# Kernel tuning notes

Measured on AMD Instinct MI355X. Metric: run time of the kernel, lower is better.

The kernel has to match this reference:

```python
import jax, jax.numpy as jnp
import numpy as np

B, C, H, W = 8, 512, 64, 64
GH, GW = 240, 240  # hardcoded grid size in the source (240*240*2 slice)


def bilinear_grid_sample(x, grid):
    """F.grid_sample equivalent: bilinear, zeros padding, align_corners=True
    (old-PyTorch default used by this repo).
    x: [b, c, H, W], grid: [b, Hg, Wg, 2] with (x, y) normalized coords in [-1, 1].
    """
    b, c, h, w = x.shape
    hg, wg = grid.shape[1], grid.shape[2]
    ix = (grid[..., 0] + 1.0) * 0.5 * (w - 1)  # unnormalize, align_corners=True
    iy = (grid[..., 1] + 1.0) * 0.5 * (h - 1)
    ix0 = jnp.floor(ix)
    iy0 = jnp.floor(iy)
    ix1 = ix0 + 1.0
    iy1 = iy0 + 1.0
    wx1 = ix - ix0
    wx0 = 1.0 - wx1
    wy1 = iy - iy0
    wy0 = 1.0 - wy1
    xf = x.transpose(0, 2, 3, 1).reshape(b, h * w, c)  # [b, HW, c]

    def gather(iy_, ix_):
        m = (iy_ >= 0) & (iy_ <= h - 1) & (ix_ >= 0) & (ix_ <= w - 1)
        iyc = jnp.clip(iy_, 0, h - 1).astype(jnp.int32)
        ixc = jnp.clip(ix_, 0, w - 1).astype(jnp.int32)
        idx = (iyc * w + ixc).reshape(b, hg * wg, 1)
        v = jnp.take_along_axis(xf, idx, axis=1).reshape(b, hg, wg, c)
        return v * m[..., None].astype(x.dtype)

    out = (gather(iy0, ix0) * (wy0 * wx0)[..., None]
           + gather(iy0, ix1) * (wy0 * wx1)[..., None]
           + gather(iy1, ix0) * (wy1 * wx0)[..., None]
           + gather(iy1, ix1) * (wy1 * wx1)[..., None])
    return out.transpose(0, 3, 1, 2)  # [b, c, Hg, Wg]


def _identity_grid(b, h, w, dtype):
    # GeometricTnf resize == grid_sample with identity affine grid (align_corners=True)
    ys = jnp.linspace(-1.0, 1.0, h, dtype=dtype)
    xs = jnp.linspace(-1.0, 1.0, w, dtype=dtype)
    gy, gx = jnp.meshgrid(ys, xs, indexing='ij')
    return jnp.broadcast_to(jnp.stack([gx, gy], axis=-1)[None], (b, h, w, 2))


def setup_inputs() -> dict:
    key = jax.random.key(0)
    # grid channels must hold normalized coords, so sample uniform in [-1, 1]
    data = jax.random.uniform(key, (B, C, H, W), dtype=jnp.float32, minval=-1.0, maxval=1.0)
    return {"data": data}


def reference(data) -> jnp.ndarray:
    b, c, h, w = data.shape
    x = data[:, :c - 256]            # [b, c-256, h, w]
    theta_aff = data[:, c - 256:c - 128]
    theta_aff_tps = data[:, c - 128:]
    g_aff = theta_aff.reshape(b, -1)[:, :GH * GW * 2].reshape(b, GH, GW, 2)
    g_tps = theta_aff_tps.reshape(b, -1)[:, :GH * GW * 2].reshape(b, GH, GW, 2)
    warped_aff = bilinear_grid_sample(x, g_aff)          # [b, cx, 240, 240]
    warped_aff_tps = bilinear_grid_sample(warped_aff, g_tps)  # [b, cx, 240, 240]
    resized = bilinear_grid_sample(warped_aff_tps, _identity_grid(b, h, w, data.dtype))
    return x + resized
```

## Files before the change

kernel.cpp:

```cpp
#include <hip/hip_runtime.h>

#define H 64
#define W 64
#define NPIX 4096
#define GHH 240
#define GWW 240
#define CB 512
#define CX 256
#define NTAP 64
#define NT4  16

static __device__ __forceinline__ unsigned pk_bf16(float a, float b) {
    unsigned ua = __float_as_uint(a);
    ua = (ua + 0x7fffu + ((ua >> 16) & 1u)) >> 16;
    unsigned ub = __float_as_uint(b);
    ub = (ub + 0x7fffu + ((ub >> 16) & 1u)) & 0xffff0000u;
    return ua | ub;
}
static __device__ __forceinline__ float lo_bf16(unsigned u) { return __uint_as_float(u << 16); }
static __device__ __forceinline__ float hi_bf16(unsigned u) { return __uint_as_float(u & 0xffff0000u); }
static __device__ __forceinline__ unsigned pk_wi(float w, unsigned idx) {
    unsigned ub = __float_as_uint(w);
    ub = (ub + 0x7fffu + ((ub >> 16) & 1u)) & 0xffff0000u;
    return ub | idx;
}

__global__ __launch_bounds__(64)
void stencil_kernel(const float* __restrict__ data, uint4* __restrict__ st) {
    const int gid = blockIdx.x * 64 + threadIdx.x;
    const int b   = gid & 7;
    const int pix = gid >> 3;
    const int oy = pix >> 6, ox = pix & 63;

    const float*  xbase = data + (size_t)b * CB * NPIX;
    const float2* gaff  = (const float2*)(xbase + (size_t)256 * NPIX);
    const float2* gtps  = (const float2*)(xbase + (size_t)384 * NPIX);
    uint4* stb = st + (size_t)b * NT4 * NPIX;

    const float fy  = ((float)oy / 63.0f) * 239.0f;
    const float fx  = ((float)ox / 63.0f) * 239.0f;
    const float fy0 = floorf(fy), fx0 = floorf(fx);
    const float wy1 = fy - fy0,  wx1 = fx - fx0;

#pragma unroll
    for (int t = 0; t < 4; ++t) {
        const int tty = t >> 1, ttx = t & 1;
        const float gyf = fy0 + (float)tty;
        const float gxf = fx0 + (float)ttx;
        float wt = (tty ? wy1 : 1.0f - wy1) * (ttx ? wx1 : 1.0f - wx1);
        if (gyf < 0.0f || gyf > 239.0f || gxf < 0.0f || gxf > 239.0f) wt = 0.0f;
        const int gyi = min(max((int)gyf, 0), GHH - 1);
        const int gxi = min(max((int)gxf, 0), GWW - 1);

        const float2 gt = gtps[gyi * GWW + gxi];
        const float sx  = (gt.x + 1.0f) * 0.5f * 239.0f;
        const float sy  = (gt.y + 1.0f) * 0.5f * 239.0f;
        const float sy0 = floorf(sy), sx0 = floorf(sx);
        const float wsy1 = sy - sy0,  wsx1 = sx - sx0;

#pragma unroll
        for (int s = 0; s < 4; ++s) {
            const int ssy = s >> 1, ssx = s & 1;
            const float ayf = sy0 + (float)ssy;
            const float axf = sx0 + (float)ssx;
            float ws = (ssy ? wsy1 : 1.0f - wsy1) * (ssx ? wsx1 : 1.0f - wsx1);
            if (ayf < 0.0f || ayf > 239.0f || axf < 0.0f || axf > 239.0f) ws = 0.0f;
            ws *= wt;
            const int ayi = min(max((int)ayf, 0), GHH - 1);
            const int axi = min(max((int)axf, 0), GWW - 1);

            const float2 ga = gaff[ayi * GWW + axi];
            const float qx  = (ga.x + 1.0f) * 0.5f * 63.0f;
            const float qy  = (ga.y + 1.0f) * 0.5f * 63.0f;
            const float qy0 = floorf(qy), qx0 = floorf(qx);
            const float wqy1 = qy - qy0,  wqx1 = qx - qx0;

            unsigned pk[4];
#pragma unroll
            for (int r = 0; r < 4; ++r) {
                const int rry = r >> 1, rrx = r & 1;
                const float byf = qy0 + (float)rry;
                const float bxf = qx0 + (float)rrx;
                float wr = (rry ? wqy1 : 1.0f - wqy1) * (rrx ? wqx1 : 1.0f - wqx1);
                if (byf < 0.0f || byf > 63.0f || bxf < 0.0f || bxf > 63.0f) wr = 0.0f;
                wr *= ws;
                const int byi = min(max((int)byf, 0), H - 1);
                const int bxi = min(max((int)bxf, 0), W - 1);
                pk[r] = pk_wi(wr, (unsigned)(byi * W + bxi));
            }
            stb[(size_t)(t * 4 + s) * NPIX + pix] = make_uint4(pk[0], pk[1], pk[2], pk[3]);
        }
    }
}

__global__ __launch_bounds__(1024)
void gather_kernel(const float* __restrict__ data, const uint4* __restrict__ st,
                   float* __restrict__ out) {
    __shared__ uint4 xl[NPIX];
    const int tid  = threadIdx.x;
    const int b    = blockIdx.x & 7;
    const int cg   = (blockIdx.x >> 3) & 31;
    const int half = blockIdx.x >> 8;
    const int c0   = cg * 8;

    const float* xbase = data + (size_t)b * CB * NPIX;
    const float* xc    = xbase + (size_t)c0 * NPIX;

#pragma unroll
    for (int k = 0; k < 4; ++k) {
        const int p = k * 1024 + tid;
        float v0 = xc[0 * NPIX + p], v1 = xc[1 * NPIX + p];
        float v2 = xc[2 * NPIX + p], v3 = xc[3 * NPIX + p];
        float v4 = xc[4 * NPIX + p], v5 = xc[5 * NPIX + p];
        float v6 = xc[6 * NPIX + p], v7 = xc[7 * NPIX + p];
        uint4 u;
        u.x = pk_bf16(v0, v1); u.y = pk_bf16(v2, v3);
        u.z = pk_bf16(v4, v5); u.w = pk_bf16(v6, v7);
        xl[p] = u;
    }
    __syncthreads();

    const uint4* stb = st + (size_t)b * NT4 * NPIX;

#pragma unroll
    for (int pg = 0; pg < 2; ++pg) {
        const int pix = half * 2048 + pg * 1024 + tid;
        float a0 = 0.f, a1 = 0.f, a2 = 0.f, a3 = 0.f;
        float a4 = 0.f, a5 = 0.f, a6 = 0.f, a7 = 0.f;

#pragma unroll 4
        for (int g = 0; g < NT4; ++g) {
            const uint4 s4 = stb[(size_t)g * NPIX + pix];
#pragma unroll
            for (int r = 0; r < 4; ++r) {
                const unsigned u = (&s4.x)[r];
                const float w = __uint_as_float(u & 0xffff0000u);
                const uint4 v = xl[u & 0xffffu];
                a0 = fmaf(w, lo_bf16(v.x), a0); a1 = fmaf(w, hi_bf16(v.x), a1);
                a2 = fmaf(w, lo_bf16(v.y), a2); a3 = fmaf(w, hi_bf16(v.y), a3);
                a4 = fmaf(w, lo_bf16(v.z), a4); a5 = fmaf(w, hi_bf16(v.z), a5);
                a6 = fmaf(w, lo_bf16(v.w), a6); a7 = fmaf(w, hi_bf16(v.w), a7);
            }
        }

        float* o = out + ((size_t)b * CX + c0) * NPIX + pix;
        o[0 * NPIX] = xc[0 * NPIX + pix] + a0;
        o[1 * NPIX] = xc[1 * NPIX + pix] + a1;
        o[2 * NPIX] = xc[2 * NPIX + pix] + a2;
        o[3 * NPIX] = xc[3 * NPIX + pix] + a3;
        o[4 * NPIX] = xc[4 * NPIX + pix] + a4;
        o[5 * NPIX] = xc[5 * NPIX + pix] + a5;
        o[6 * NPIX] = xc[6 * NPIX + pix] + a6;
        o[7 * NPIX] = xc[7 * NPIX + pix] + a7;
    }
}

__global__ __launch_bounds__(1024, 4)
void warp_resblock_mono(const float* __restrict__ data, float* __restrict__ out) {
    const int tid = threadIdx.x;
    const int b   = blockIdx.x & 7;
    const int cg  = blockIdx.x >> 3;
    const int c0  = cg * 8;

    const float*  xbase = data + (size_t)b * CB * NPIX;
    const float2* gaff  = (const float2*)(xbase + (size_t)256 * NPIX);
    const float2* gtps  = (const float2*)(xbase + (size_t)384 * NPIX);

    __shared__ float4 xa[NPIX];
    __shared__ float4 xb[NPIX];
    {
        const float4* xs = (const float4*)(xbase + (size_t)c0 * NPIX);
        float4 va[4], vb[4];
#pragma unroll
        for (int cc = 0; cc < 4; ++cc) va[cc] = xs[(size_t)cc * 1024 + tid];
#pragma unroll
        for (int cc = 0; cc < 4; ++cc) vb[cc] = xs[(size_t)(4 + cc) * 1024 + tid];
#pragma unroll
        for (int k = 0; k < 4; ++k) {
            const int pix = tid * 4 + k;
            xa[pix] = make_float4(((const float*)&va[0])[k], ((const float*)&va[1])[k],
                                  ((const float*)&va[2])[k], ((const float*)&va[3])[k]);
            xb[pix] = make_float4(((const float*)&vb[0])[k], ((const float*)&vb[1])[k],
                                  ((const float*)&vb[2])[k], ((const float*)&vb[3])[k]);
        }
    }
    __syncthreads();

    for (int pg = 0; pg < 4; ++pg) {
        const int pix = pg * 1024 + tid;
        const int oy = pix >> 6, ox = pix & 63;
        float a0 = 0.f, a1 = 0.f, a2 = 0.f, a3 = 0.f;
        float a4 = 0.f, a5 = 0.f, a6 = 0.f, a7 = 0.f;

        const float fy  = ((float)oy / 63.0f) * 239.0f;
        const float fx  = ((float)ox / 63.0f) * 239.0f;
        const float fy0 = floorf(fy), fx0 = floorf(fx);
        const float wy1 = fy - fy0,  wx1 = fx - fx0;

#pragma unroll
        for (int t = 0; t < 4; ++t) {
            const int tty = t >> 1, ttx = t & 1;
            const float gyf = fy0 + (float)tty;
            const float gxf = fx0 + (float)ttx;
            float wt = (tty ? wy1 : 1.0f - wy1) * (ttx ? wx1 : 1.0f - wx1);
            if (gyf < 0.0f || gyf > 239.0f || gxf < 0.0f || gxf > 239.0f) wt = 0.0f;
            const int gyi = min(max((int)gyf, 0), GHH - 1);
            const int gxi = min(max((int)gxf, 0), GWW - 1);
            const float2 gt = gtps[gyi * GWW + gxi];
            const float sx  = (gt.x + 1.0f) * 0.5f * 239.0f;
            const float sy  = (gt.y + 1.0f) * 0.5f * 239.0f;
            const float sy0 = floorf(sy), sx0 = floorf(sx);
            const float wsy1 = sy - sy0,  wsx1 = sx - sx0;
#pragma unroll
            for (int s = 0; s < 4; ++s) {
                const int ssy = s >> 1, ssx = s & 1;
                const float ayf = sy0 + (float)ssy;
                const float axf = sx0 + (float)ssx;
                float ws = (ssy ? wsy1 : 1.0f - wsy1) * (ssx ? wsx1 : 1.0f - wsx1);
                if (ayf < 0.0f || ayf > 239.0f || axf < 0.0f || axf > 239.0f) ws = 0.0f;
                ws *= wt;
                const int ayi = min(max((int)ayf, 0), GHH - 1);
                const int axi = min(max((int)axf, 0), GWW - 1);
                const float2 ga = gaff[ayi * GWW + axi];
                const float qx  = (ga.x + 1.0f) * 0.5f * 63.0f;
                const float qy  = (ga.y + 1.0f) * 0.5f * 63.0f;
                const float qy0 = floorf(qy), qx0 = floorf(qx);
                const float wqy1 = qy - qy0,  wqx1 = qx - qx0;
#pragma unroll
                for (int r = 0; r < 4; ++r) {
                    const int rry = r >> 1, rrx = r & 1;
                    const float byf = qy0 + (float)rry;
                    const float bxf = qx0 + (float)rrx;
                    float wr = (rry ? wqy1 : 1.0f - wqy1) * (rrx ? wqx1 : 1.0f - wqx1);
                    if (byf < 0.0f || byf > 63.0f || bxf < 0.0f || bxf > 63.0f) wr = 0.0f;
                    wr *= ws;
                    const int byi = min(max((int)byf, 0), H - 1);
                    const int bxi = min(max((int)bxf, 0), W - 1);
                    const int idx = byi * W + bxi;
                    const float4 pa = xa[idx];
                    const float4 pb = xb[idx];
                    a0 = fmaf(wr, pa.x, a0); a1 = fmaf(wr, pa.y, a1);
                    a2 = fmaf(wr, pa.z, a2); a3 = fmaf(wr, pa.w, a3);
                    a4 = fmaf(wr, pb.x, a4); a5 = fmaf(wr, pb.y, a5);
                    a6 = fmaf(wr, pb.z, a6); a7 = fmaf(wr, pb.w, a7);
                }
            }
        }
        const float4 ra = xa[pix];
        const float4 rb = xb[pix];
        float* o = out + ((size_t)b * CX + c0) * NPIX + pix;
        o[0 * NPIX] = ra.x + a0; o[1 * NPIX] = ra.y + a1;
        o[2 * NPIX] = ra.z + a2; o[3 * NPIX] = ra.w + a3;
        o[4 * NPIX] = rb.x + a4; o[5 * NPIX] = rb.y + a5;
        o[6 * NPIX] = rb.z + a6; o[7 * NPIX] = rb.w + a7;
    }
}

extern "C" void kernel_launch(void* const* d_in, const int* in_sizes, int n_in,
                              void* d_out, int out_size, void* d_ws, size_t ws_size,
                              hipStream_t stream) {
    (void)in_sizes; (void)n_in; (void)out_size;
    const float* data = (const float*)d_in[0];
    float* out = (float*)d_out;
    const size_t ws_needed = (size_t)8 * NT4 * NPIX * sizeof(uint4);

    if (ws_size >= ws_needed) {
        uint4* st = (uint4*)d_ws;
        hipLaunchKernelGGL(stencil_kernel, dim3(512), dim3(64), 0, stream, data, st);
        hipLaunchKernelGGL(gather_kernel, dim3(512), dim3(1024), 0, stream, data, st, out);
    } else {
        hipLaunchKernelGGL(warp_resblock_mono, dim3(256), dim3(1024), 0, stream, data, out);
    }
}
```

Before: 53.44 us.

## Vectorize gather loads, process two pixels per thread, nontemporal stores

The stencil kernel moves to 256-thread blocks with each block covering one batch. The gather kernel now loads channel data with float4 vector reads when filling LDS, and each thread accumulates two adjacent pixels at once, which doubles independent LDS gathers in flight. Outputs are written as float2 nontemporal stores, and a launch bound hints at 8 waves per SIMD. The goal is more memory-level parallelism and wider transactions. In exchange, register pressure rises from 16 accumulators, and the stencil loads become strided by two pixels.

New measurement: 55.19 us. 1.03x slower.

```diff
diff --git a/kernel.cpp b/kernel.cpp
--- a/kernel.cpp
+++ b/kernel.cpp
@@ -7,8 +7,9 @@
 #define GWW 240
 #define CB 512
 #define CX 256
-#define NTAP 64
 #define NT4  16
+
+typedef float f32x2 __attribute__((ext_vector_type(2)));
 
 static __device__ __forceinline__ unsigned pk_bf16(float a, float b) {
     unsigned ua = __float_as_uint(a);
@@ -25,11 +26,10 @@
     return ub | idx;
 }
 
-__global__ __launch_bounds__(64)
+__global__ __launch_bounds__(256)
 void stencil_kernel(const float* __restrict__ data, uint4* __restrict__ st) {
-    const int gid = blockIdx.x * 64 + threadIdx.x;
-    const int b   = gid & 7;
-    const int pix = gid >> 3;
+    const int b   = blockIdx.x & 7;
+    const int pix = (blockIdx.x >> 3) * 256 + threadIdx.x;
     const int oy = pix >> 6, ox = pix & 63;
 
     const float*  xbase = data + (size_t)b * CB * NPIX;
@@ -93,7 +93,7 @@
     }
 }
 
-__global__ __launch_bounds__(1024)
+__global__ __launch_bounds__(1024, 8)
 void gather_kernel(const float* __restrict__ data, const uint4* __restrict__ st,
                    float* __restrict__ out) {
     __shared__ uint4 xl[NPIX];
@@ -106,52 +106,61 @@
     const float* xbase = data + (size_t)b * CB * NPIX;
     const float* xc    = xbase + (size_t)c0 * NPIX;
 
-#pragma unroll
-    for (int k = 0; k < 4; ++k) {
-        const int p = k * 1024 + tid;
-        float v0 = xc[0 * NPIX + p], v1 = xc[1 * NPIX + p];
-        float v2 = xc[2 * NPIX + p], v3 = xc[3 * NPIX + p];
-        float v4 = xc[4 * NPIX + p], v5 = xc[5 * NPIX + p];
-        float v6 = xc[6 * NPIX + p], v7 = xc[7 * NPIX + p];
-        uint4 u;
-        u.x = pk_bf16(v0, v1); u.y = pk_bf16(v2, v3);
-        u.z = pk_bf16(v4, v5); u.w = pk_bf16(v6, v7);
-        xl[p] = u;
+    {
+        float4 va[8];
+#pragma unroll
+        for (int c = 0; c < 8; ++c)
+            va[c] = ((const float4*)(xc + (size_t)c * NPIX))[tid];
+#pragma unroll
+        for (int k = 0; k < 4; ++k) {
+            uint4 u;
+            u.x = pk_bf16(((const float*)&va[0])[k], ((const float*)&va[1])[k]);
+            u.y = pk_bf16(((const float*)&va[2])[k], ((const float*)&va[3])[k]);
+            u.z = pk_bf16(((const float*)&va[4])[k], ((const float*)&va[5])[k]);
+            u.w = pk_bf16(((const float*)&va[6])[k], ((const float*)&va[7])[k]);
+            xl[tid * 4 + k] = u;
+        }
     }
     __syncthreads();
 
     const uint4* stb = st + (size_t)b * NT4 * NPIX;
-
-#pragma unroll
-    for (int pg = 0; pg < 2; ++pg) {
-        const int pix = half * 2048 + pg * 1024 + tid;
-        float a0 = 0.f, a1 = 0.f, a2 = 0.f, a3 = 0.f;
-        float a4 = 0.f, a5 = 0.f, a6 = 0.f, a7 = 0.f;
+    const int pix0 = half * 2048 + tid * 2;
+
+    float a0[8], a1[8];
+#pragma unroll
+    for (int c = 0; c < 8; ++c) { a0[c] = 0.f; a1[c] = 0.f; }
 
 #pragma unroll 4
-        for (int g = 0; g < NT4; ++g) {
-            const uint4 s4 = stb[(size_t)g * NPIX + pix];
-#pragma unroll
-            for (int r = 0; r < 4; ++r) {
-                const unsigned u = (&s4.x)[r];
-                const float w = __uint_as_float(u & 0xffff0000u);
-                const uint4 v = xl[u & 0xffffu];
-                a0 = fmaf(w, lo_bf16(v.x), a0); a1 = fmaf(w, hi_bf16(v.x), a1);
-                a2 = fmaf(w, lo_bf16(v.y), a2); a3 = fmaf(w, hi_bf16(v.y), a3);
-                a4 = fmaf(w, lo_bf16(v.z), a4); a5 = fmaf(w, hi_bf16(v.z), a5);
-                a6 = fmaf(w, lo_bf16(v.w), a6); a7 = fmaf(w, hi_bf16(v.w), a7);
-            }
-        }
-
-        float* o = out + ((size_t)b * CX + c0) * NPIX + pix;
-        o[0 * NPIX] = xc[0 * NPIX + pix] + a0;
-        o[1 * NPIX] = xc[1 * NPIX + pix] + a1;
-        o[2 * NPIX] = xc[2 * NPIX + pix] + a2;
-        o[3 * NPIX] = xc[3 * NPIX + pix] + a3;
-        o[4 * NPIX] = xc[4 * NPIX + pix] + a4;
-        o[5 * NPIX] = xc[5 * NPIX + pix] + a5;
-        o[6 * NPIX] = xc[6 * NPIX + pix] + a6;
-        o[7 * NPIX] = xc[7 * NPIX + pix] + a7;
+    for (int g = 0; g < NT4; ++g) {
+        const uint4 sa = stb[(size_t)g * NPIX + pix0];
+        const uint4 sb = stb[(size_t)g * NPIX + pix0 + 1];
+#pragma unroll
+        for (int r = 0; r < 4; ++r) {
+            const unsigned ua = (&sa.x)[r];
+            const unsigned ub = (&sb.x)[r];
+            const float wa = __uint_as_float(ua & 0xffff0000u);
+            const float wb = __uint_as_float(ub & 0xffff0000u);
+            const uint4 va = xl[ua & 0xffffu];
+            const uint4 vb = xl[ub & 0xffffu];
+            a0[0] = fmaf(wa, lo_bf16(va.x), a0[0]); a1[0] = fmaf(wb, lo_bf16(vb.x), a1[0]);
+            a0[1] = fmaf(wa, hi_bf16(va.x), a0[1]); a1[1] = fmaf(wb, hi_bf16(vb.x), a1[1]);
+            a0[2] = fmaf(wa, lo_bf16(va.y), a0[2]); a1[2] = fmaf(wb, lo_bf16(vb.y), a1[2]);
+            a0[3] = fmaf(wa, hi_bf16(va.y), a0[3]); a1[3] = fmaf(wb, hi_bf16(vb.y), a1[3]);
+            a0[4] = fmaf(wa, lo_bf16(va.z), a0[4]); a1[4] = fmaf(wb, lo_bf16(vb.z), a1[4]);
+            a0[5] = fmaf(wa, hi_bf16(va.z), a0[5]); a1[5] = fmaf(wb, hi_bf16(vb.z), a1[5]);
+            a0[6] = fmaf(wa, lo_bf16(va.w), a0[6]); a1[6] = fmaf(wb, lo_bf16(vb.w), a1[6]);
+            a0[7] = fmaf(wa, hi_bf16(va.w), a0[7]); a1[7] = fmaf(wb, hi_bf16(vb.w), a1[7]);
+        }
+    }
+
+#pragma unroll
+    for (int c = 0; c < 8; ++c) {
+        const float2 rv = ((const float2*)(xc + (size_t)c * NPIX))[pix0 >> 1];
+        f32x2 ov;
+        ov.x = rv.x + a0[c];
+        ov.y = rv.y + a1[c];
+        f32x2* op = (f32x2*)(out + ((size_t)b * CX + c0 + c) * NPIX + pix0);
+        __builtin_nontemporal_store(ov, op);
     }
 }
 
@@ -266,7 +275,7 @@
 
     if (ws_size >= ws_needed) {
         uint4* st = (uint4*)d_ws;
-        hipLaunchKernelGGL(stencil_kernel, dim3(512), dim3(64), 0, stream, data, st);
+        hipLaunchKernelGGL(stencil_kernel, dim3(128), dim3(256), 0, stream, data, st);
         hipLaunchKernelGGL(gather_kernel, dim3(512), dim3(1024), 0, stream, data, st, out);
     } else {
         hipLaunchKernelGGL(warp_resblock_mono, dim3(256), dim3(1024), 0, stream, data, out);
```

## Use fp16 LDS staging with vectorized loads and retile stencil launch

Applied to the files above, without the earlier changes.

The gather kernel now stages the 8-channel input slice in shared memory as packed fp16 instead of bf16. It fills that staging buffer with float4 vector loads, so each thread packs four consecutive pixels. The stencil kernel moves from 64-thread to 256-thread blocks, with the batch index taken from the block index, which changes its memory access pattern. The gather kernel also gets a higher occupancy hint in launch_bounds. fp16 keeps more mantissa than bf16, and the half-to-float conversions may cost slightly more per tap than shift/mask unpacking.

Measured after the change: 52.98 us. No clear change (-0.9%).

```diff
diff --git a/kernel.cpp b/kernel.cpp
--- a/kernel.cpp
+++ b/kernel.cpp
@@ -1,4 +1,5 @@
 #include <hip/hip_runtime.h>
+#include <hip/hip_fp16.h>
 
 #define H 64
 #define W 64
@@ -7,29 +8,22 @@
 #define GWW 240
 #define CB 512
 #define CX 256
-#define NTAP 64
 #define NT4  16
 
-static __device__ __forceinline__ unsigned pk_bf16(float a, float b) {
-    unsigned ua = __float_as_uint(a);
-    ua = (ua + 0x7fffu + ((ua >> 16) & 1u)) >> 16;
-    unsigned ub = __float_as_uint(b);
-    ub = (ub + 0x7fffu + ((ub >> 16) & 1u)) & 0xffff0000u;
-    return ua | ub;
-}
-static __device__ __forceinline__ float lo_bf16(unsigned u) { return __uint_as_float(u << 16); }
-static __device__ __forceinline__ float hi_bf16(unsigned u) { return __uint_as_float(u & 0xffff0000u); }
 static __device__ __forceinline__ unsigned pk_wi(float w, unsigned idx) {
     unsigned ub = __float_as_uint(w);
     ub = (ub + 0x7fffu + ((ub >> 16) & 1u)) & 0xffff0000u;
     return ub | idx;
 }
-
-__global__ __launch_bounds__(64)
+static __device__ __forceinline__ unsigned pk_f16(float a, float b) {
+    __half2 h = __floats2half2_rn(a, b);
+    return *reinterpret_cast<unsigned*>(&h);
+}
+
+__global__ __launch_bounds__(256)
 void stencil_kernel(const float* __restrict__ data, uint4* __restrict__ st) {
-    const int gid = blockIdx.x * 64 + threadIdx.x;
-    const int b   = gid & 7;
-    const int pix = gid >> 3;
+    const int b   = blockIdx.x & 7;
+    const int pix = (blockIdx.x >> 3) * 256 + threadIdx.x;
     const int oy = pix >> 6, ox = pix & 63;
 
     const float*  xbase = data + (size_t)b * CB * NPIX;
@@ -93,7 +87,7 @@
     }
 }
 
-__global__ __launch_bounds__(1024)
+__global__ __launch_bounds__(1024, 8)
 void gather_kernel(const float* __restrict__ data, const uint4* __restrict__ st,
                    float* __restrict__ out) {
     __shared__ uint4 xl[NPIX];
@@ -106,17 +100,20 @@
     const float* xbase = data + (size_t)b * CB * NPIX;
     const float* xc    = xbase + (size_t)c0 * NPIX;
 
-#pragma unroll
-    for (int k = 0; k < 4; ++k) {
-        const int p = k * 1024 + tid;
-        float v0 = xc[0 * NPIX + p], v1 = xc[1 * NPIX + p];
-        float v2 = xc[2 * NPIX + p], v3 = xc[3 * NPIX + p];
-        float v4 = xc[4 * NPIX + p], v5 = xc[5 * NPIX + p];
-        float v6 = xc[6 * NPIX + p], v7 = xc[7 * NPIX + p];
-        uint4 u;
-        u.x = pk_bf16(v0, v1); u.y = pk_bf16(v2, v3);
-        u.z = pk_bf16(v4, v5); u.w = pk_bf16(v6, v7);
-        xl[p] = u;
+    {
+        float4 va[8];
+#pragma unroll
+        for (int c = 0; c < 8; ++c)
+            va[c] = ((const float4*)(xc + (size_t)c * NPIX))[tid];
+#pragma unroll
+        for (int k = 0; k < 4; ++k) {
+            uint4 u;
+            u.x = pk_f16(((const float*)&va[0])[k], ((const float*)&va[1])[k]);
+            u.y = pk_f16(((const float*)&va[2])[k], ((const float*)&va[3])[k]);
+            u.z = pk_f16(((const float*)&va[4])[k], ((const float*)&va[5])[k]);
+            u.w = pk_f16(((const float*)&va[6])[k], ((const float*)&va[7])[k]);
+            xl[tid * 4 + k] = u;
+        }
     }
     __syncthreads();
 
@@ -136,10 +133,18 @@
                 const unsigned u = (&s4.x)[r];
                 const float w = __uint_as_float(u & 0xffff0000u);
                 const uint4 v = xl[u & 0xffffu];
-                a0 = fmaf(w, lo_bf16(v.x), a0); a1 = fmaf(w, hi_bf16(v.x), a1);
-                a2 = fmaf(w, lo_bf16(v.y), a2); a3 = fmaf(w, hi_bf16(v.y), a3);
-                a4 = fmaf(w, lo_bf16(v.z), a4); a5 = fmaf(w, hi_bf16(v.z), a5);
-                a6 = fmaf(w, lo_bf16(v.w), a6); a7 = fmaf(w, hi_bf16(v.w), a7);
+                const __half2 h01 = *reinterpret_cast<const __half2*>(&v.x);
+                const __half2 h23 = *reinterpret_cast<const __half2*>(&v.y);
+                const __half2 h45 = *reinterpret_cast<const __half2*>(&v.z);
+                const __half2 h67 = *reinterpret_cast<const __half2*>(&v.w);
+                a0 = fmaf(w, __half2float(__low2half (h01)), a0);
+                a1 = fmaf(w, __half2float(__high2half(h01)), a1);
+                a2 = fmaf(w, __half2float(__low2half (h23)), a2);
+                a3 = fmaf(w, __half2float(__high2half(h23)), a3);
+                a4 = fmaf(w, __half2float(__low2half (h45)), a4);
+                a5 = fmaf(w, __half2float(__high2half(h45)), a5);
+                a6 = fmaf(w, __half2float(__low2half (h67)), a6);
+                a7 = fmaf(w, __half2float(__high2half(h67)), a7);
             }
         }
 
@@ -266,7 +271,7 @@
 
     if (ws_size >= ws_needed) {
         uint4* st = (uint4*)d_ws;
-        hipLaunchKernelGGL(stencil_kernel, dim3(512), dim3(64), 0, stream, data, st);
+        hipLaunchKernelGGL(stencil_kernel, dim3(128), dim3(256), 0, stream, data, st);
         hipLaunchKernelGGL(gather_kernel, dim3(512), dim3(1024), 0, stream, data, st, out);
     } else {
         hipLaunchKernelGGL(warp_resblock_mono, dim3(256), dim3(1024), 0, stream, data, out);
```
